# Kernel optimization log

Measured on AMD Instinct MI355X. Metric: run time of the kernel, lower is better.

Reference implementation:

```python
import jax, jax.numpy as jnp
import numpy as np

N = 100000
E = 3200000
IN_DIM, HID, MLP_HID, K = 3, 64, 128, 15


def setup_inputs() -> dict:
    key = jax.random.key(0)
    ks = jax.random.split(key, 10)
    x = jax.random.normal(ks[0], (N, IN_DIM), dtype=jnp.float32)
    edge_index = jax.random.randint(ks[1], (2, E), 0, N, dtype=jnp.int32)
    def glorot(k, shape):
        lim = float(np.sqrt(6.0 / (shape[0] + shape[1])))
        return jax.random.uniform(k, shape, jnp.float32, -lim, lim)
    return {
        "x": x,
        "edge_index": edge_index,
        "W1": glorot(ks[2], (IN_DIM, HID)), "b1": jnp.zeros((HID,), jnp.float32),
        "W2": glorot(ks[3], (HID, HID)),    "b2": jnp.zeros((HID,), jnp.float32),
        "Wm1": glorot(ks[4], (HID, MLP_HID)), "bm1": jnp.zeros((MLP_HID,), jnp.float32),
        "Wm2": glorot(ks[5], (MLP_HID, K)),   "bm2": jnp.zeros((K,), jnp.float32),
    }


def _gcn_layer(h, W, b, src, dst, deg_inv_sqrt, n):
    # h: [N, Fin] -> [N, Fout]; GCNConv: D^-1/2 (A+I) D^-1/2 (h W) + b
    hw = h @ W  # dense GEMM first (Fin small)
    norm = deg_inv_sqrt[src] * deg_inv_sqrt[dst]  # [E+N]
    msg = hw[src] * norm[:, None]                 # irregular gather, [E+N, Fout]
    out = jax.ops.segment_sum(msg, dst, num_segments=n)  # scatter-add
    return out + b


def reference(x, edge_index, W1, b1, W2, b2, Wm1, bm1, Wm2, bm2):
    n = x.shape[0]
    loops = jnp.arange(n, dtype=edge_index.dtype)
    src = jnp.concatenate([edge_index[0], loops])  # self-loops appended
    dst = jnp.concatenate([edge_index[1], loops])
    deg = jax.ops.segment_sum(jnp.ones_like(dst, dtype=x.dtype), dst, num_segments=n)
    deg_inv_sqrt = jnp.where(deg > 0, jax.lax.rsqrt(jnp.maximum(deg, 1.0)), 0.0)

    h = jax.nn.elu(_gcn_layer(x, W1, b1, src, dst, deg_inv_sqrt, n))
    h = jax.nn.elu(_gcn_layer(h, W2, b2, src, dst, deg_inv_sqrt, n))
    # MLP (dropout is identity in eval mode)
    h = jax.nn.elu(h @ Wm1 + bm1)
    H = h @ Wm2 + bm2
    return jax.nn.softmax(H, axis=1)  # [N, K]
```

## Files before the change

### kernel.cpp

```cpp
#include <hip/hip_runtime.h>
#include <hip/hip_fp16.h>
#include <math.h>


#define SPAN 128
#define CAP  4608
#define CH   8192
#define H2P  88
#define MSP2 136

typedef _Float16 v8hf __attribute__((ext_vector_type(8)));
typedef float    v4f  __attribute__((ext_vector_type(4)));

__device__ __forceinline__ float elu(float v) { return v > 0.f ? v : expm1f(v); }

__global__ __launch_bounds__(256) void scatter_kernel(const int* __restrict__ src,
    const int* __restrict__ dst, int* __restrict__ cursor, unsigned* __restrict__ colb,
    int E, int NBK, int nChunks) {
    __shared__ int hist[1024];
    __shared__ unsigned gb[1024];
    int tid = threadIdx.x;
    for (int chunk = blockIdx.x; chunk < nChunks; chunk += gridDim.x) {
        for (int i = tid; i < NBK; i += 256) hist[i] = 0;
        __syncthreads();
        int base = chunk * CH;
        int cnt = min(CH, E - base);
        unsigned br[32], dt[32];
#pragma unroll
        for (int j = 0; j < 32; ++j) {
            int idx = j * 256 + tid;
            br[j] = 0xFFFFFFFFu;
            if (idx < cnt) {
                int e = base + idx;
                int s = src[e], d = dst[e];
                int b = d >> 7;
                int r = atomicAdd(&hist[b], 1);
                br[j] = ((unsigned)b << 13) | (unsigned)r;
                dt[j] = ((unsigned)(d & 127) << 17) | (unsigned)s;
            }
        }
        __syncthreads();
        for (int b = tid; b < NBK; b += 256) {
            int c = hist[b];
            gb[b] = (unsigned)(b * CAP) + (c ? (unsigned)atomicAdd(&cursor[b], c) : 0u);
        }
        __syncthreads();
#pragma unroll
        for (int j = 0; j < 32; ++j) {
            if (br[j] != 0xFFFFFFFFu) {
                int b = br[j] >> 13;
                int r = br[j] & 8191;
                unsigned pos = gb[b] + (unsigned)r;
                if (pos < (unsigned)(b + 1) * CAP) colb[pos] = dt[j];
            }
        }
        __syncthreads();
    }
}

__global__ __launch_bounds__(1024) void bscan_kernel(const int* __restrict__ cursor,
    int* __restrict__ bbase, int* __restrict__ row_ptr, int NBK, int N) {
    __shared__ int ls[1024];
    int t = threadIdx.x;
    int v = (t < NBK) ? min(cursor[t], CAP) : 0;
    ls[t] = v;
    __syncthreads();
    for (int off = 1; off < 1024; off <<= 1) {
        int xv = (t >= off) ? ls[t - off] : 0;
        __syncthreads();
        ls[t] += xv;
        __syncthreads();
    }
    if (t < NBK) bbase[t] = ls[t] - v;
    if (t == NBK - 1) row_ptr[N] = ls[t];
}

__global__ __launch_bounds__(256) void csr_sort_kernel(const unsigned* __restrict__ colb,
    const int* __restrict__ cursor, const int* __restrict__ bbase,
    const float* __restrict__ x, int* __restrict__ row_ptr, int* __restrict__ col,
    float* __restrict__ dis, float4* __restrict__ sx4, int N) {
    __shared__ unsigned ebuf[CAP];
    __shared__ int sbuf[CAP];
    __shared__ int cnt[SPAN], pref[SPAN], fill[SPAN];
    int b = blockIdx.x, tid = threadIdx.x;
    int n = min(cursor[b], CAP);
    int base = b * CAP, bb = bbase[b];
    if (tid < SPAN) cnt[tid] = 0;
    for (int i = tid; i < n; i += 256) ebuf[i] = colb[base + i];
    __syncthreads();
    for (int i = tid; i < n; i += 256) atomicAdd(&cnt[(ebuf[i] >> 17) & 127], 1);
    __syncthreads();
    if (tid < SPAN) pref[tid] = cnt[tid];
    __syncthreads();
    for (int off = 1; off < SPAN; off <<= 1) {
        int xv = (tid < SPAN && tid >= off) ? pref[tid - off] : 0;
        __syncthreads();
        if (tid < SPAN) pref[tid] += xv;
        __syncthreads();
    }
    if (tid < SPAN) {
        int ex = pref[tid] - cnt[tid];
        fill[tid] = ex;
        int node = b * SPAN + tid;
        if (node < N) {
            row_ptr[node] = bb + ex;
            float r = rsqrtf((float)(cnt[tid] + 1));
            dis[node] = r;
            float4 q;
            q.x = r * x[node * 3 + 0];
            q.y = r * x[node * 3 + 1];
            q.z = r * x[node * 3 + 2];
            q.w = 0.f;
            sx4[node] = q;
        }
    }
    __syncthreads();
    for (int i = tid; i < n; i += 256) {
        unsigned e = ebuf[i];
        int pos = atomicAdd(&fill[(e >> 17) & 127], 1);
        sbuf[pos] = (int)(e & 0x1FFFF);
    }
    __syncthreads();
    for (int i = tid; i < n; i += 256) col[bb + i] = sbuf[i];
}

__global__ void agg3_kernel(const float4* __restrict__ sx4, const int* __restrict__ row_ptr,
                            const int* __restrict__ col, const float* __restrict__ dis,
                            const float* __restrict__ W1, const float* __restrict__ b1,
                            __half* __restrict__ s1h, int N) {
    int wave = (blockIdx.x * blockDim.x + threadIdx.x) >> 6;
    int lane = threadIdx.x & 63;
    if (wave >= N) return;
    int d = wave;
    int start = row_ptr[d], end = row_ptr[d + 1];
    float a0 = 0.f, a1 = 0.f, a2v = 0.f;
    for (int i = start + lane; i < end; i += 64) {
        float4 q = sx4[col[i]];
        a0 += q.x; a1 += q.y; a2v += q.z;
    }
#pragma unroll
    for (int off = 32; off; off >>= 1) {
        a0  += __shfl_xor(a0, off);
        a1  += __shfl_xor(a1, off);
        a2v += __shfl_xor(a2v, off);
    }
    float4 qd = sx4[d];
    a0 += qd.x; a1 += qd.y; a2v += qd.z;
    float r = dis[d];
    float v = r * (a0 * W1[lane] + a1 * W1[64 + lane] + a2v * W1[128 + lane]) + b1[lane];
    s1h[(size_t)d * 64 + lane] = __float2half(r * elu(v));
}

__global__ void agg64_kernel(const __half2* __restrict__ s1h, const int* __restrict__ row_ptr,
                             const int* __restrict__ col, const float* __restrict__ dis,
                             __half2* __restrict__ a2h, int N) {
    int wave = (blockIdx.x * blockDim.x + threadIdx.x) >> 6;
    int lane = threadIdx.x & 63;
    int hl = lane & 31;
    int d = wave * 2 + (lane >> 5);
    bool act = d < N;
    int start = 0, end = 0;
    if (act) { start = row_ptr[d]; end = row_ptr[d + 1]; }
    float a0x = 0.f, a0y = 0.f, a1x = 0.f, a1y = 0.f;
    float a2x = 0.f, a2y = 0.f, a3x = 0.f, a3y = 0.f;
    float a4x = 0.f, a4y = 0.f, a5x = 0.f, a5y = 0.f;
    float a6x = 0.f, a6y = 0.f, a7x = 0.f, a7y = 0.f;
    if (act) {
        float2 v = __half22float2(s1h[(size_t)d * 32 + hl]);
        a0x = v.x; a0y = v.y;
    }
    int i = start;
    for (; i + 7 < end; i += 8) {
        int c0 = col[i],     c1 = col[i + 1], c2 = col[i + 2], c3 = col[i + 3];
        int c4 = col[i + 4], c5 = col[i + 5], c6 = col[i + 6], c7 = col[i + 7];
        float2 v0 = __half22float2(s1h[(size_t)c0 * 32 + hl]);
        float2 v1 = __half22float2(s1h[(size_t)c1 * 32 + hl]);
        float2 v2 = __half22float2(s1h[(size_t)c2 * 32 + hl]);
        float2 v3 = __half22float2(s1h[(size_t)c3 * 32 + hl]);
        float2 v4 = __half22float2(s1h[(size_t)c4 * 32 + hl]);
        float2 v5 = __half22float2(s1h[(size_t)c5 * 32 + hl]);
        float2 v6 = __half22float2(s1h[(size_t)c6 * 32 + hl]);
        float2 v7 = __half22float2(s1h[(size_t)c7 * 32 + hl]);
        a0x += v0.x; a0y += v0.y; a1x += v1.x; a1y += v1.y;
        a2x += v2.x; a2y += v2.y; a3x += v3.x; a3y += v3.y;
        a4x += v4.x; a4y += v4.y; a5x += v5.x; a5y += v5.y;
        a6x += v6.x; a6y += v6.y; a7x += v7.x; a7y += v7.y;
    }
    for (; i < end; ++i) {
        float2 v = __half22float2(s1h[(size_t)col[i] * 32 + hl]);
        a0x += v.x; a0y += v.y;
    }
    if (act) {
        float r = dis[d];
        float ox = r * (((a0x + a1x) + (a2x + a3x)) + ((a4x + a5x) + (a6x + a7x)));
        float oy = r * (((a0y + a1y) + (a2y + a3y)) + ((a4y + a5y) + (a6y + a7y)));
        a2h[(size_t)d * 32 + hl] = __floats2half2_rn(ox, oy);
    }
}

__global__ __launch_bounds__(256) void prep_kernel(const float* __restrict__ W2,
    const float* __restrict__ Wm1, __half* __restrict__ W2t, __half* __restrict__ Wm1t) {
    int tid = blockIdx.x * 256 + threadIdx.x;
    if (tid < 64 * 64) {
        int f = tid >> 6, k = tid & 63;
        W2t[f * 64 + k] = __float2half(W2[k * 64 + f]);
    }
    if (tid < 128 * 64) {
        int j = tid >> 6, f = tid & 63;
        Wm1t[j * 64 + f] = __float2half(Wm1[f * 128 + j]);
    }
}

__global__ __launch_bounds__(256) void h1_kernel(const __half* __restrict__ a2h,
    const __half* __restrict__ W2t, const float* __restrict__ b2g,
    const __half* __restrict__ Wm1t, const float* __restrict__ bm1g,
    __half* __restrict__ m, int N) {
    __shared__ __align__(16) __half h2s[64 * H2P];
    __shared__ __align__(16) __half ms[64 * MSP2];
    __shared__ float b2s[64], bm1s[128];
    int tid = threadIdx.x;
    if (tid < 64)  b2s[tid]  = b2g[tid];
    if (tid < 128) bm1s[tid] = bm1g[tid];
    __syncthreads();

    int wave = tid >> 6, lane = tid & 63;
    int q = lane >> 4, l16 = lane & 15;
    int base = blockIdx.x * 64;

    {
        int nodeRow = base + wave * 16 + l16;
        size_t arow = (size_t)min(nodeRow, N - 1) * 64;
        v8hf af0 = *(const v8hf*)(a2h + arow + q * 8);
        v8hf af1 = *(const v8hf*)(a2h + arow + 32 + q * 8);
#pragma unroll
        for (int fb = 0; fb < 4; ++fb) {
            float bb = b2s[fb * 16 + l16];
            v4f acc = {bb, bb, bb, bb};
            v8hf b0 = *(const v8hf*)(W2t + (fb * 16 + l16) * 64 + q * 8);
            v8hf b1 = *(const v8hf*)(W2t + (fb * 16 + l16) * 64 + 32 + q * 8);
            acc = __builtin_amdgcn_mfma_f32_16x16x32_f16(af0, b0, acc, 0, 0, 0);
            acc = __builtin_amdgcn_mfma_f32_16x16x32_f16(af1, b1, acc, 0, 0, 0);
#pragma unroll
            for (int r = 0; r < 4; ++r)
                h2s[(wave * 16 + q * 4 + r) * H2P + fb * 16 + l16] =
                    __float2half(elu(acc[r]));
        }
    }
    __syncthreads();
    {
        int arow = (wave * 16 + l16) * H2P;
        v8hf af0 = *(const v8hf*)(h2s + arow + q * 8);
        v8hf af1 = *(const v8hf*)(h2s + arow + 32 + q * 8);
#pragma unroll
        for (int jb = 0; jb < 8; ++jb) {
            float bb = bm1s[jb * 16 + l16];
            v4f acc = {bb, bb, bb, bb};
            v8hf b0 = *(const v8hf*)(Wm1t + (jb * 16 + l16) * 64 + q * 8);
            v8hf b1 = *(const v8hf*)(Wm1t + (jb * 16 + l16) * 64 + 32 + q * 8);
            acc = __builtin_amdgcn_mfma_f32_16x16x32_f16(af0, b0, acc, 0, 0, 0);
            acc = __builtin_amdgcn_mfma_f32_16x16x32_f16(af1, b1, acc, 0, 0, 0);
#pragma unroll
            for (int r = 0; r < 4; ++r)
                ms[(wave * 16 + q * 4 + r) * MSP2 + jb * 16 + l16] =
                    __float2half(elu(acc[r]));
        }
    }
    __syncthreads();
    for (int i = tid; i < 64 * 16; i += 256) {
        int row = i >> 4, c8 = i & 15;
        int node = base + row;
        if (node < N)
            *(float4*)(m + (size_t)node * 128 + c8 * 8) =
                *(const float4*)(ms + row * MSP2 + c8 * 8);
    }
}

__global__ __launch_bounds__(256) void h2_kernel(const __half* __restrict__ m,
    const float* __restrict__ Wm2g, const float* __restrict__ bm2g,
    float* __restrict__ out, int N) {
    __shared__ float Wt[15 * 128];
    int tid = threadIdx.x;
    for (int i = tid; i < 15 * 128; i += 256) {
        int c = i >> 7, j = i & 127;
        Wt[i] = Wm2g[j * 15 + c];
    }
    __syncthreads();
    int node = blockIdx.x * 256 + tid;
    if (node >= N) return;
    float lg[15];
#pragma unroll
    for (int c = 0; c < 15; ++c) lg[c] = bm2g[c];
    const __half* row = m + (size_t)node * 128;
#pragma unroll 2
    for (int j8 = 0; j8 < 128; j8 += 8) {
        float4 raw = *(const float4*)(row + j8);
        const __half2* hp = (const __half2*)&raw;
        float mv[8];
#pragma unroll
        for (int h = 0; h < 4; ++h) {
            float2 u = __half22float2(hp[h]);
            mv[2 * h] = u.x; mv[2 * h + 1] = u.y;
        }
#pragma unroll
        for (int c = 0; c < 15; ++c) {
            float4 w0 = *(const float4*)(Wt + c * 128 + j8);
            float4 w1 = *(const float4*)(Wt + c * 128 + j8 + 4);
            lg[c] = fmaf(mv[0], w0.x, fmaf(mv[1], w0.y, fmaf(mv[2], w0.z,
                    fmaf(mv[3], w0.w, fmaf(mv[4], w1.x, fmaf(mv[5], w1.y,
                    fmaf(mv[6], w1.z, fmaf(mv[7], w1.w, lg[c]))))))));
        }
    }
    float mx = lg[0];
#pragma unroll
    for (int c = 1; c < 15; ++c) mx = fmaxf(mx, lg[c]);
    float ex[15], s = 0.f;
#pragma unroll
    for (int c = 0; c < 15; ++c) { ex[c] = __expf(lg[c] - mx); s += ex[c]; }
    float inv = 1.f / s;
#pragma unroll
    for (int c = 0; c < 15; ++c) out[(size_t)node * 15 + c] = ex[c] * inv;
}

extern "C" void kernel_launch(void* const* d_in, const int* in_sizes, int n_in,
                              void* d_out, int out_size, void* d_ws, size_t ws_size,
                              hipStream_t stream) {
    const float* x   = (const float*)d_in[0];
    const int*   ei  = (const int*)d_in[1];
    const float* W1  = (const float*)d_in[2];
    const float* b1  = (const float*)d_in[3];
    const float* W2  = (const float*)d_in[4];
    const float* b2  = (const float*)d_in[5];
    const float* Wm1 = (const float*)d_in[6];
    const float* bm1 = (const float*)d_in[7];
    const float* Wm2 = (const float*)d_in[8];
    const float* bm2 = (const float*)d_in[9];
    float* out = (float*)d_out;

    int N = in_sizes[0] / 3;
    int E = in_sizes[1] / 2;
    const int* src = ei;
    const int* dst = ei + E;
    int NBK = (N + SPAN - 1) / SPAN;

    uintptr_t p = (uintptr_t)d_ws;
    auto carve = [&](size_t bytes) -> void* {
        p = (p + 255) & ~(uintptr_t)255;
        void* r = (void*)p;
        p += bytes;
        return r;
    };
    __half*   a2h     = (__half*)carve((size_t)N * 64 * 2);
    __half*   m       = (__half*)carve((size_t)N * 128 * 2);
    int*      cursor  = (int*)carve((size_t)NBK * 4);
    int*      bbase   = (int*)carve((size_t)NBK * 4);
    int*      row_ptr = (int*)carve((size_t)(N + 1) * 4);
    float*    dis     = (float*)carve((size_t)N * 4);
    float4*   sx4     = (float4*)carve((size_t)N * 16);
    int*      col     = (int*)carve((size_t)E * 4);
    __half*   s1h     = (__half*)carve((size_t)N * 64 * 2);
    __half*   W2t     = (__half*)carve(64 * 64 * 2);
    __half*   Wm1t    = (__half*)carve(128 * 64 * 2);
    unsigned* colb = (unsigned*)m;

    hipMemsetAsync(cursor, 0, (size_t)NBK * 4, stream);

    int nChunks = (E + CH - 1) / CH;
    int waveBlocks3  = (N + 3) / 4;
    int waveBlocks64 = (N + 7) / 8;
    int nTiles = (N + 63) / 64;
    scatter_kernel<<<nChunks, 256, 0, stream>>>(src, dst, cursor, colb, E, NBK, nChunks);
    bscan_kernel<<<1, 1024, 0, stream>>>(cursor, bbase, row_ptr, NBK, N);
    prep_kernel<<<32, 256, 0, stream>>>(W2, Wm1, W2t, Wm1t);
    csr_sort_kernel<<<NBK, 256, 0, stream>>>(colb, cursor, bbase, x, row_ptr, col, dis, sx4, N);
    agg3_kernel<<<waveBlocks3, 256, 0, stream>>>(sx4, row_ptr, col, dis, W1, b1, s1h, N);
    agg64_kernel<<<waveBlocks64, 256, 0, stream>>>((const __half2*)s1h, row_ptr, col, dis,
                                                   (__half2*)a2h, N);
    h1_kernel<<<nTiles, 256, 0, stream>>>(a2h, W2t, b2, Wm1t, bm1, m, N);
    h2_kernel<<<(N + 255) / 256, 256, 0, stream>>>(m, Wm2, bm2, out, N);
}
```

Baseline: 273.3 us.

## Fuse MLP output layer into h1, drop scan/memset kernels, repack gathers

Several changes land at once. The final Wm2 matmul and softmax move into h1_kernel, so the 128-wide fp16 intermediate never goes through global memory. The block scan kernel and memset are removed: cursor zeroing goes into prep_kernel, and each csr_sort block recomputes its base by summing earlier bucket counts. The scatter chunk size is halved, with one chunk per block. x is packed as fp16 (8 bytes per node instead of 16), and agg64 now gathers 8-byte vectors with two neighbours per half-wave, pre-adding in half precision. Risks are fp16 precision loss on the pre-add, and redundant prefix sums that grow with the block index in csr_sort.

```diff
diff --git a/kernel.cpp b/kernel.cpp
--- a/kernel.cpp
+++ b/kernel.cpp
@@ -5,7 +5,8 @@
 
 #define SPAN 128
 #define CAP  4608
-#define CH   8192
+#define CH   4096
+#define EPT  16
 #define H2P  88
 #define MSP2 136
 
@@ -14,80 +15,85 @@
 
 __device__ __forceinline__ float elu(float v) { return v > 0.f ? v : expm1f(v); }
 
+__global__ __launch_bounds__(256) void prep_kernel(const float* __restrict__ W2,
+    const float* __restrict__ Wm1, __half* __restrict__ W2t, __half* __restrict__ Wm1t,
+    int* __restrict__ cursor, int NBK) {
+    int tid = blockIdx.x * 256 + threadIdx.x;
+    if (tid < NBK) cursor[tid] = 0;
+    if (tid < 64 * 64) {
+        int f = tid >> 6, k = tid & 63;
+        W2t[f * 64 + k] = __float2half(W2[k * 64 + f]);
+    }
+    if (tid < 128 * 64) {
+        int j = tid >> 6, f = tid & 63;
+        Wm1t[j * 64 + f] = __float2half(Wm1[f * 128 + j]);
+    }
+}
+
 __global__ __launch_bounds__(256) void scatter_kernel(const int* __restrict__ src,
     const int* __restrict__ dst, int* __restrict__ cursor, unsigned* __restrict__ colb,
-    int E, int NBK, int nChunks) {
+    int E, int NBK) {
     __shared__ int hist[1024];
     __shared__ unsigned gb[1024];
     int tid = threadIdx.x;
-    for (int chunk = blockIdx.x; chunk < nChunks; chunk += gridDim.x) {
-        for (int i = tid; i < NBK; i += 256) hist[i] = 0;
-        __syncthreads();
-        int base = chunk * CH;
-        int cnt = min(CH, E - base);
-        unsigned br[32], dt[32];
-#pragma unroll
-        for (int j = 0; j < 32; ++j) {
-            int idx = j * 256 + tid;
-            br[j] = 0xFFFFFFFFu;
-            if (idx < cnt) {
-                int e = base + idx;
-                int s = src[e], d = dst[e];
-                int b = d >> 7;
-                int r = atomicAdd(&hist[b], 1);
-                br[j] = ((unsigned)b << 13) | (unsigned)r;
-                dt[j] = ((unsigned)(d & 127) << 17) | (unsigned)s;
-            }
-        }
-        __syncthreads();
-        for (int b = tid; b < NBK; b += 256) {
-            int c = hist[b];
-            gb[b] = (unsigned)(b * CAP) + (c ? (unsigned)atomicAdd(&cursor[b], c) : 0u);
-        }
-        __syncthreads();
-#pragma unroll
-        for (int j = 0; j < 32; ++j) {
-            if (br[j] != 0xFFFFFFFFu) {
-                int b = br[j] >> 13;
-                int r = br[j] & 8191;
-                unsigned pos = gb[b] + (unsigned)r;
-                if (pos < (unsigned)(b + 1) * CAP) colb[pos] = dt[j];
-            }
-        }
-        __syncthreads();
-    }
-}
-
-__global__ __launch_bounds__(1024) void bscan_kernel(const int* __restrict__ cursor,
-    int* __restrict__ bbase, int* __restrict__ row_ptr, int NBK, int N) {
-    __shared__ int ls[1024];
-    int t = threadIdx.x;
-    int v = (t < NBK) ? min(cursor[t], CAP) : 0;
-    ls[t] = v;
-    __syncthreads();
-    for (int off = 1; off < 1024; off <<= 1) {
-        int xv = (t >= off) ? ls[t - off] : 0;
-        __syncthreads();
-        ls[t] += xv;
-        __syncthreads();
-    }
-    if (t < NBK) bbase[t] = ls[t] - v;
-    if (t == NBK - 1) row_ptr[N] = ls[t];
+    int chunk = blockIdx.x;
+    for (int i = tid; i < NBK; i += 256) hist[i] = 0;
+    __syncthreads();
+    int base = chunk * CH;
+    int cnt = min(CH, E - base);
+    unsigned br[EPT], dt[EPT];
+#pragma unroll
+    for (int j = 0; j < EPT; ++j) {
+        int idx = j * 256 + tid;
+        br[j] = 0xFFFFFFFFu;
+        if (idx < cnt) {
+            int e = base + idx;
+            int s = src[e], d = dst[e];
+            int b = d >> 7;
+            int r = atomicAdd(&hist[b], 1);
+            br[j] = ((unsigned)b << 13) | (unsigned)r;
+            dt[j] = ((unsigned)(d & 127) << 17) | (unsigned)s;
+        }
+    }
+    __syncthreads();
+    for (int b = tid; b < NBK; b += 256) {
+        int c = hist[b];
+        gb[b] = (unsigned)(b * CAP) + (c ? (unsigned)atomicAdd(&cursor[b], c) : 0u);
+    }
+    __syncthreads();
+#pragma unroll
+    for (int j = 0; j < EPT; ++j) {
+        if (br[j] != 0xFFFFFFFFu) {
+            int b = br[j] >> 13;
+            int r = br[j] & 8191;
+            unsigned pos = gb[b] + (unsigned)r;
+            if (pos < (unsigned)(b + 1) * CAP) colb[pos] = dt[j];
+        }
+    }
 }
 
 __global__ __launch_bounds__(256) void csr_sort_kernel(const unsigned* __restrict__ colb,
-    const int* __restrict__ cursor, const int* __restrict__ bbase,
-    const float* __restrict__ x, int* __restrict__ row_ptr, int* __restrict__ col,
-    float* __restrict__ dis, float4* __restrict__ sx4, int N) {
+    const int* __restrict__ cursor, const float* __restrict__ x,
+    int* __restrict__ row_ptr, int* __restrict__ col,
+    float* __restrict__ dis, __half* __restrict__ sxh, int N, int NBK) {
     __shared__ unsigned ebuf[CAP];
     __shared__ int sbuf[CAP];
     __shared__ int cnt[SPAN], pref[SPAN], fill[SPAN];
+    __shared__ int redbuf[256];
     int b = blockIdx.x, tid = threadIdx.x;
     int n = min(cursor[b], CAP);
-    int base = b * CAP, bb = bbase[b];
+    int base = b * CAP;
+    int partial = 0;
+    for (int i2 = tid; i2 < b; i2 += 256) partial += min(cursor[i2], CAP);
+    redbuf[tid] = partial;
     if (tid < SPAN) cnt[tid] = 0;
     for (int i = tid; i < n; i += 256) ebuf[i] = colb[base + i];
     __syncthreads();
+    for (int off = 128; off; off >>= 1) {
+        if (tid < off) redbuf[tid] += redbuf[tid + off];
+        __syncthreads();
+    }
+    int bb = redbuf[0];
     for (int i = tid; i < n; i += 256) atomicAdd(&cnt[(ebuf[i] >> 17) & 127], 1);
     __syncthreads();
     if (tid < SPAN) pref[tid] = cnt[tid];
@@ -106,14 +112,13 @@
             row_ptr[node] = bb + ex;
             float r = rsqrtf((float)(cnt[tid] + 1));
             dis[node] = r;
-            float4 q;
-            q.x = r * x[node * 3 + 0];
-            q.y = r * x[node * 3 + 1];
-            q.z = r * x[node * 3 + 2];
-            q.w = 0.f;
-            sx4[node] = q;
-        }
-    }
+            __half2 h0 = __floats2half2_rn(r * x[node * 3 + 0], r * x[node * 3 + 1]);
+            __half2 h1 = __floats2half2_rn(r * x[node * 3 + 2], 0.f);
+            uint2 w; w.x = *(unsigned*)&h0; w.y = *(unsigned*)&h1;
+            *(uint2*)(sxh + (size_t)node * 4) = w;
+        }
+    }
+    if (b == NBK - 1 && tid == 0) row_ptr[N] = bb + n;
     __syncthreads();
     for (int i = tid; i < n; i += 256) {
         unsigned e = ebuf[i];
@@ -124,7 +129,7 @@
     for (int i = tid; i < n; i += 256) col[bb + i] = sbuf[i];
 }
 
-__global__ void agg3_kernel(const float4* __restrict__ sx4, const int* __restrict__ row_ptr,
+__global__ void agg3_kernel(const __half* __restrict__ sxh, const int* __restrict__ row_ptr,
                             const int* __restrict__ col, const float* __restrict__ dis,
                             const float* __restrict__ W1, const float* __restrict__ b1,
                             __half* __restrict__ s1h, int N) {
@@ -135,8 +140,10 @@
     int start = row_ptr[d], end = row_ptr[d + 1];
     float a0 = 0.f, a1 = 0.f, a2v = 0.f;
     for (int i = start + lane; i < end; i += 64) {
-        float4 q = sx4[col[i]];
-        a0 += q.x; a1 += q.y; a2v += q.z;
+        uint2 rq = *(const uint2*)(sxh + (size_t)col[i] * 4);
+        float2 u0 = __half22float2(*(__half2*)&rq.x);
+        float2 u1 = __half22float2(*(__half2*)&rq.y);
+        a0 += u0.x; a1 += u0.y; a2v += u1.x;
     }
 #pragma unroll
     for (int off = 32; off; off >>= 1) {
@@ -144,83 +151,87 @@
         a1  += __shfl_xor(a1, off);
         a2v += __shfl_xor(a2v, off);
     }
-    float4 qd = sx4[d];
-    a0 += qd.x; a1 += qd.y; a2v += qd.z;
+    {
+        uint2 rq = *(const uint2*)(sxh + (size_t)d * 4);
+        float2 u0 = __half22float2(*(__half2*)&rq.x);
+        float2 u1 = __half22float2(*(__half2*)&rq.y);
+        a0 += u0.x; a1 += u0.y; a2v += u1.x;
+    }
     float r = dis[d];
     float v = r * (a0 * W1[lane] + a1 * W1[64 + lane] + a2v * W1[128 + lane]) + b1[lane];
     s1h[(size_t)d * 64 + lane] = __float2half(r * elu(v));
 }
 
-__global__ void agg64_kernel(const __half2* __restrict__ s1h, const int* __restrict__ row_ptr,
+__global__ void agg64_kernel(const __half* __restrict__ s1h, const int* __restrict__ row_ptr,
                              const int* __restrict__ col, const float* __restrict__ dis,
-                             __half2* __restrict__ a2h, int N) {
+                             __half* __restrict__ a2h, int N) {
     int wave = (blockIdx.x * blockDim.x + threadIdx.x) >> 6;
     int lane = threadIdx.x & 63;
     int hl = lane & 31;
+    int sub = hl >> 4;
+    int fl  = hl & 15;
     int d = wave * 2 + (lane >> 5);
     bool act = d < N;
     int start = 0, end = 0;
     if (act) { start = row_ptr[d]; end = row_ptr[d + 1]; }
-    float a0x = 0.f, a0y = 0.f, a1x = 0.f, a1y = 0.f;
-    float a2x = 0.f, a2y = 0.f, a3x = 0.f, a3y = 0.f;
-    float a4x = 0.f, a4y = 0.f, a5x = 0.f, a5y = 0.f;
-    float a6x = 0.f, a6y = 0.f, a7x = 0.f, a7y = 0.f;
-    if (act) {
-        float2 v = __half22float2(s1h[(size_t)d * 32 + hl]);
-        a0x = v.x; a0y = v.y;
-    }
+    float ax = 0.f, ay = 0.f, az = 0.f, aw = 0.f;
     int i = start;
     for (; i + 7 < end; i += 8) {
-        int c0 = col[i],     c1 = col[i + 1], c2 = col[i + 2], c3 = col[i + 3];
-        int c4 = col[i + 4], c5 = col[i + 5], c6 = col[i + 6], c7 = col[i + 7];
-        float2 v0 = __half22float2(s1h[(size_t)c0 * 32 + hl]);
-        float2 v1 = __half22float2(s1h[(size_t)c1 * 32 + hl]);
-        float2 v2 = __half22float2(s1h[(size_t)c2 * 32 + hl]);
-        float2 v3 = __half22float2(s1h[(size_t)c3 * 32 + hl]);
-        float2 v4 = __half22float2(s1h[(size_t)c4 * 32 + hl]);
-        float2 v5 = __half22float2(s1h[(size_t)c5 * 32 + hl]);
-        float2 v6 = __half22float2(s1h[(size_t)c6 * 32 + hl]);
-        float2 v7 = __half22float2(s1h[(size_t)c7 * 32 + hl]);
-        a0x += v0.x; a0y += v0.y; a1x += v1.x; a1y += v1.y;
-        a2x += v2.x; a2y += v2.y; a3x += v3.x; a3y += v3.y;
-        a4x += v4.x; a4y += v4.y; a5x += v5.x; a5y += v5.y;
-        a6x += v6.x; a6y += v6.y; a7x += v7.x; a7y += v7.y;
+#pragma unroll
+        for (int qq = 0; qq < 2; ++qq) {
+            int c0 = col[i + 4 * qq + sub];
+            int c1 = col[i + 4 * qq + 2 + sub];
+            uint2 r0 = *(const uint2*)(s1h + (size_t)c0 * 64 + fl * 4);
+            uint2 r1 = *(const uint2*)(s1h + (size_t)c1 * 64 + fl * 4);
+            __half2 p0 = __hadd2(*(__half2*)&r0.x, *(__half2*)&r1.x);
+            __half2 p1 = __hadd2(*(__half2*)&r0.y, *(__half2*)&r1.y);
+            float2 u0 = __half22float2(p0);
+            float2 u1 = __half22float2(p1);
+            ax += u0.x; ay += u0.y; az += u1.x; aw += u1.y;
+        }
     }
     for (; i < end; ++i) {
-        float2 v = __half22float2(s1h[(size_t)col[i] * 32 + hl]);
-        a0x += v.x; a0y += v.y;
-    }
-    if (act) {
-        float r = dis[d];
-        float ox = r * (((a0x + a1x) + (a2x + a3x)) + ((a4x + a5x) + (a6x + a7x)));
-        float oy = r * (((a0y + a1y) + (a2y + a3y)) + ((a4y + a5y) + (a6y + a7y)));
-        a2h[(size_t)d * 32 + hl] = __floats2half2_rn(ox, oy);
-    }
-}
-
-__global__ __launch_bounds__(256) void prep_kernel(const float* __restrict__ W2,
-    const float* __restrict__ Wm1, __half* __restrict__ W2t, __half* __restrict__ Wm1t) {
-    int tid = blockIdx.x * 256 + threadIdx.x;
-    if (tid < 64 * 64) {
-        int f = tid >> 6, k = tid & 63;
-        W2t[f * 64 + k] = __float2half(W2[k * 64 + f]);
-    }
-    if (tid < 128 * 64) {
-        int j = tid >> 6, f = tid & 63;
-        Wm1t[j * 64 + f] = __float2half(Wm1[f * 128 + j]);
+        if (sub == 0) {
+            uint2 r0 = *(const uint2*)(s1h + (size_t)col[i] * 64 + fl * 4);
+            float2 u0 = __half22float2(*(__half2*)&r0.x);
+            float2 u1 = __half22float2(*(__half2*)&r0.y);
+            ax += u0.x; ay += u0.y; az += u1.x; aw += u1.y;
+        }
+    }
+    ax += __shfl_xor(ax, 16);
+    ay += __shfl_xor(ay, 16);
+    az += __shfl_xor(az, 16);
+    aw += __shfl_xor(aw, 16);
+    if (act && sub == 0) {
+        uint2 r0 = *(const uint2*)(s1h + (size_t)d * 64 + fl * 4);
+        float2 u0 = __half22float2(*(__half2*)&r0.x);
+        float2 u1 = __half22float2(*(__half2*)&r0.y);
+        float rd = dis[d];
+        __half2 o0 = __floats2half2_rn(rd * (ax + u0.x), rd * (ay + u0.y));
+        __half2 o1 = __floats2half2_rn(rd * (az + u1.x), rd * (aw + u1.y));
+        uint2 w; w.x = *(unsigned*)&o0; w.y = *(unsigned*)&o1;
+        *(uint2*)(a2h + (size_t)d * 64 + fl * 4) = w;
     }
 }
 
 __global__ __launch_bounds__(256) void h1_kernel(const __half* __restrict__ a2h,
     const __half* __restrict__ W2t, const float* __restrict__ b2g,
     const __half* __restrict__ Wm1t, const float* __restrict__ bm1g,
-    __half* __restrict__ m, int N) {
+    const float* __restrict__ Wm2g, const float* __restrict__ bm2g,
+    float* __restrict__ out, int N) {
     __shared__ __align__(16) __half h2s[64 * H2P];
     __shared__ __align__(16) __half ms[64 * MSP2];
-    __shared__ float b2s[64], bm1s[128];
+    __shared__ float Wt2[15 * 128];
+    __shared__ float lgs[16 * 16];
+    __shared__ float b2s[64], bm1s[128], bm2s[16];
     int tid = threadIdx.x;
     if (tid < 64)  b2s[tid]  = b2g[tid];
     if (tid < 128) bm1s[tid] = bm1g[tid];
+    if (tid < 16)  bm2s[tid] = (tid < 15) ? bm2g[tid] : 0.f;
+    for (int i = tid; i < 15 * 128; i += 256) {
+        int c = i >> 7, j = i & 127;
+        Wt2[i] = Wm2g[j * 15 + c];
+    }
     __syncthreads();
 
     int wave = tid >> 6, lane = tid & 63;
@@ -266,59 +277,39 @@
         }
     }
     __syncthreads();
-    for (int i = tid; i < 64 * 16; i += 256) {
-        int row = i >> 4, c8 = i & 15;
-        int node = base + row;
-        if (node < N)
-            *(float4*)(m + (size_t)node * 128 + c8 * 8) =
-                *(const float4*)(ms + row * MSP2 + c8 * 8);
-    }
-}
-
-__global__ __launch_bounds__(256) void h2_kernel(const __half* __restrict__ m,
-    const float* __restrict__ Wm2g, const float* __restrict__ bm2g,
-    float* __restrict__ out, int N) {
-    __shared__ float Wt[15 * 128];
-    int tid = threadIdx.x;
-    for (int i = tid; i < 15 * 128; i += 256) {
-        int c = i >> 7, j = i & 127;
-        Wt[i] = Wm2g[j * 15 + c];
-    }
-    __syncthreads();
-    int node = blockIdx.x * 256 + tid;
-    if (node >= N) return;
-    float lg[15];
-#pragma unroll
-    for (int c = 0; c < 15; ++c) lg[c] = bm2g[c];
-    const __half* row = m + (size_t)node * 128;
-#pragma unroll 2
-    for (int j8 = 0; j8 < 128; j8 += 8) {
-        float4 raw = *(const float4*)(row + j8);
-        const __half2* hp = (const __half2*)&raw;
-        float mv[8];
-#pragma unroll
-        for (int h = 0; h < 4; ++h) {
-            float2 u = __half22float2(hp[h]);
-            mv[2 * h] = u.x; mv[2 * h + 1] = u.y;
-        }
-#pragma unroll
-        for (int c = 0; c < 15; ++c) {
-            float4 w0 = *(const float4*)(Wt + c * 128 + j8);
-            float4 w1 = *(const float4*)(Wt + c * 128 + j8 + 4);
-            lg[c] = fmaf(mv[0], w0.x, fmaf(mv[1], w0.y, fmaf(mv[2], w0.z,
-                    fmaf(mv[3], w0.w, fmaf(mv[4], w1.x, fmaf(mv[5], w1.y,
-                    fmaf(mv[6], w1.z, fmaf(mv[7], w1.w, lg[c]))))))));
-        }
-    }
-    float mx = lg[0];
-#pragma unroll
-    for (int c = 1; c < 15; ++c) mx = fmaxf(mx, lg[c]);
-    float ex[15], s = 0.f;
-#pragma unroll
-    for (int c = 0; c < 15; ++c) { ex[c] = __expf(lg[c] - mx); s += ex[c]; }
-    float inv = 1.f / s;
-#pragma unroll
-    for (int c = 0; c < 15; ++c) out[(size_t)node * 15 + c] = ex[c] * inv;
+    {
+        int cc = tid % 15;
+        int nn = tid / 15;
+        bool actC = tid < 240;
+#pragma unroll
+        for (int it = 0; it < 4; ++it) {
+            if (actC) {
+                int row = it * 16 + nn;
+                float acc = bm2s[cc];
+                const __half2* mrow = (const __half2*)(ms + row * MSP2);
+                const float* wrow = Wt2 + cc * 128;
+#pragma unroll 4
+                for (int j2 = 0; j2 < 64; ++j2) {
+                    float2 u = __half22float2(mrow[j2]);
+                    acc = fmaf(u.x, wrow[2 * j2], fmaf(u.y, wrow[2 * j2 + 1], acc));
+                }
+                lgs[nn * 16 + cc] = acc;
+            }
+            __syncthreads();
+            if (actC) {
+                int node = base + it * 16 + nn;
+                float mx = lgs[nn * 16 + 0];
+#pragma unroll
+                for (int c2 = 1; c2 < 15; ++c2) mx = fmaxf(mx, lgs[nn * 16 + c2]);
+                float sden = 0.f;
+#pragma unroll
+                for (int c2 = 0; c2 < 15; ++c2) sden += __expf(lgs[nn * 16 + c2] - mx);
+                if (node < N)
+                    out[(size_t)node * 15 + cc] = __expf(lgs[nn * 16 + cc] - mx) / sden;
+            }
+            __syncthreads();
+        }
+    }
 }
 
 extern "C" void kernel_launch(void* const* d_in, const int* in_sizes, int n_in,
@@ -350,31 +341,24 @@
         return r;
     };
     __half*   a2h     = (__half*)carve((size_t)N * 64 * 2);
-    __half*   m       = (__half*)carve((size_t)N * 128 * 2);
+    __half*   s1h     = (__half*)carve((size_t)N * 64 * 2);
     int*      cursor  = (int*)carve((size_t)NBK * 4);
-    int*      bbase   = (int*)carve((size_t)NBK * 4);
     int*      row_ptr = (int*)carve((size_t)(N + 1) * 4);
     float*    dis     = (float*)carve((size_t)N * 4);
-    float4*   sx4     = (float4*)carve((size_t)N * 16);
+    __half*   sxh     = (__half*)carve((size_t)N * 8);
     int*      col     = (int*)carve((size_t)E * 4);
-    __half*   s1h     = (__half*)carve((size_t)N * 64 * 2);
     __half*   W2t     = (__half*)carve(64 * 64 * 2);
     __half*   Wm1t    = (__half*)carve(128 * 64 * 2);
-    unsigned* colb = (unsigned*)m;
-
-    hipMemsetAsync(cursor, 0, (size_t)NBK * 4, stream);
+    unsigned* colb = (unsigned*)a2h;
 
     int nChunks = (E + CH - 1) / CH;
     int waveBlocks3  = (N + 3) / 4;
     int waveBlocks64 = (N + 7) / 8;
     int nTiles = (N + 63) / 64;
-    scatter_kernel<<<nChunks, 256, 0, stream>>>(src, dst, cursor, colb, E, NBK, nChunks);
-    bscan_kernel<<<1, 1024, 0, stream>>>(cursor, bbase, row_ptr, NBK, N);
-    prep_kernel<<<32, 256, 0, stream>>>(W2, Wm1, W2t, Wm1t);
-    csr_sort_kernel<<<NBK, 256, 0, stream>>>(colb, cursor, bbase, x, row_ptr, col, dis, sx4, N);
-    agg3_kernel<<<waveBlocks3, 256, 0, stream>>>(sx4, row_ptr, col, dis, W1, b1, s1h, N);
-    agg64_kernel<<<waveBlocks64, 256, 0, stream>>>((const __half2*)s1h, row_ptr, col, dis,
-                                                   (__half2*)a2h, N);
-    h1_kernel<<<nTiles, 256, 0, stream>>>(a2h, W2t, b2, Wm1t, bm1, m, N);
-    h2_kernel<<<(N + 255) / 256, 256, 0, stream>>>(m, Wm2, bm2, out, N);
-}
+    prep_kernel<<<32, 256, 0, stream>>>(W2, Wm1, W2t, Wm1t, cursor, NBK);
+    scatter_kernel<<<nChunks, 256, 0, stream>>>(src, dst, cursor, colb, E, NBK);
+    csr_sort_kernel<<<NBK, 256, 0, stream>>>(colb, cursor, x, row_ptr, col, dis, sxh, N, NBK);
+    agg3_kernel<<<waveBlocks3, 256, 0, stream>>>(sxh, row_ptr, col, dis, W1, b1, s1h, N);
+    agg64_kernel<<<waveBlocks64, 256, 0, stream>>>(s1h, row_ptr, col, dis, a2h, N);
+    h1_kernel<<<nTiles, 256, 0, stream>>>(a2h, W2t, b2, Wm1t, bm1, Wm2, bm2, out, N);
+}
```

Measured after the change: 337.1 us. 1.23x slower.
